# Kernel tuning notes

Hardware: AMD Instinct MI355X
Metric: run time of the kernel (lower is better)

## Reference

```python
import jax, jax.numpy as jnp
import numpy as np

ALPHA = 0.2          # LeakyReLU negative slope
NEG_BIG = -9e15      # mask value from original code


def setup_inputs() -> dict:
    key = jax.random.key(0)
    k1, k2, k3, k4 = jax.random.split(key, 4)
    B, N, F_in, F_out = 16, 1024, 256, 256
    x = jax.random.normal(k1, (B, N, F_in), dtype=jnp.float32)
    adj = jax.random.randint(k2, (B, N, N), 0, 2, dtype=jnp.int32)
    # xavier-uniform-like scales
    W = jax.random.normal(k3, (F_in, F_out), dtype=jnp.float32) * np.sqrt(2.0 / (F_in + F_out))
    a = jax.random.normal(k4, (2 * F_out, 1), dtype=jnp.float32) * np.sqrt(2.0 / (2 * F_out + 1))
    return {"x": x, "adj": adj, "W": W, "a": a}


def reference(x, adj, W, a):
    # x: [B,N,Fin], adj: [B,N,N] (int mask), W: [Fin,Fout], a: [2*Fout,1]
    F_out = a.shape[0] // 2
    h = jnp.einsum("bni,io->bno", x, W)            # [B,N,Fout]
    # Decompose a into left/right halves: e_ij = lrelu(a_l.h_i + a_r.h_j)
    a_l = a[:F_out, 0]                               # [Fout]
    a_r = a[F_out:, 0]                               # [Fout]
    el = h @ a_l                                     # [B,N] score contribution of target i
    er = h @ a_r                                     # [B,N] score contribution of source j
    e = jax.nn.leaky_relu(el[:, :, None] + er[:, None, :], ALPHA)  # [B,N,N]
    e = jnp.where(adj > 0, e, NEG_BIG)
    attn = jax.nn.softmax(e, axis=-1)                # masked softmax over neighbors j
    # weighted sum of neighbor features; concat with n_heads=1 is identity
    return jnp.einsum("bij,bjo->bio", attn, h)       # [B,N,Fout]
```

## Files before the change

kernel.cpp:

```cpp
#include <hip/hip_runtime.h>
#include <stdint.h>

#define ALPHA 0.2f
#define L2E 1.4426950408889634f

typedef __attribute__((ext_vector_type(8))) short bf16x8;
typedef __attribute__((ext_vector_type(4))) float f32x4;

__device__ __forceinline__ unsigned short f2bf(float f) {
    unsigned int u = __float_as_uint(f);
    u += 0x7fffu + ((u >> 16) & 1u);
    return (unsigned short)(u >> 16);
}

__device__ __forceinline__ void gload_lds16(const void* g, void* l) {
    __builtin_amdgcn_global_load_lds(
        (const __attribute__((address_space(1))) unsigned int*)g,
        (__attribute__((address_space(3))) unsigned int*)l, 16, 0, 0);
}

__global__ void wt_wa_kernel(const float* __restrict__ W,
                             const float* __restrict__ a,
                             unsigned short* __restrict__ Wtbf,
                             float* __restrict__ wa) {
    const int t = threadIdx.x;
    if (blockIdx.x < 256) {
        const int o = blockIdx.x;
        Wtbf[o * 256 + t] = f2bf(W[t * 256 + o]);
    } else {
        float sl = 0.f, sr = 0.f;
        const float* wr = W + t * 256;
        for (int o = 0; o < 256; ++o) {
            const float wv = wr[o];
            sl += wv * a[o];
            sr += wv * a[256 + o];
        }
        wa[t] = sl;
        wa[256 + t] = sr;
    }
}

__global__ __launch_bounds__(256) void eler2x_kernel(
    const float* __restrict__ x, const float* __restrict__ wa,
    float* __restrict__ el, float* __restrict__ er,
    unsigned short* __restrict__ xbf)
{
    const int w = threadIdx.x >> 6, l = threadIdx.x & 63;
    const int r = blockIdx.x * 4 + w;
    const float4 xv = *(const float4*)(x + (size_t)r * 256 + l * 4);
    const float4 al = *(const float4*)(wa + l * 4);
    const float4 ar = *(const float4*)(wa + 256 + l * 4);

    ushort4 xb;
    xb.x = f2bf(xv.x); xb.y = f2bf(xv.y); xb.z = f2bf(xv.z); xb.w = f2bf(xv.w);
    *(ushort4*)(xbf + (size_t)r * 256 + l * 4) = xb;

    float sl = xv.x * al.x + xv.y * al.y + xv.z * al.z + xv.w * al.w;
    float sr = xv.x * ar.x + xv.y * ar.y + xv.z * ar.z + xv.w * ar.w;
#pragma unroll
    for (int off = 32; off >= 1; off >>= 1) {
        sl += __shfl_xor(sl, off);
        sr += __shfl_xor(sr, off);
    }
    if (l == 0) { el[r] = sl * L2E; er[r] = sr * L2E; }
}

__global__ __launch_bounds__(256) void gemm_h(
    const unsigned short* __restrict__ A,
    const unsigned short* __restrict__ Bt,
    unsigned short* __restrict__ C)
{
    __shared__ __align__(16) unsigned short As[2 * 64 * 64];
    __shared__ __align__(16) unsigned short Bs[2 * 128 * 64];

    const int tid = threadIdx.x;
    const int w = tid >> 6, l = tid & 63;
    const int q = l >> 4, ml = l & 15;
    const int wm = (w >> 1) * 32;
    const int wn = (w & 1) * 64;
    const int m0 = blockIdx.y * 64;
    const int n0 = blockIdx.x * 128;

    f32x4 acc[2][4];
#pragma unroll
    for (int i = 0; i < 2; ++i)
#pragma unroll
        for (int j = 0; j < 4; ++j) {
            f32x4 z = {0.f, 0.f, 0.f, 0.f};
            acc[i][j] = z;
        }

#define GSTAGE(BI, K0) do {                                                   \
    _Pragma("unroll")                                                         \
    for (int c_ = 0; c_ < 2; ++c_) {                                          \
        const int cb_ = c_ * 256 + (w << 6);                                  \
        const int p_ = cb_ + l;                                               \
        const int r_ = p_ >> 3;                                               \
        const int cc_ = (p_ & 7) ^ (r_ & 7);                                  \
        gload_lds16(A + (size_t)(m0 + r_) * 256 + (K0) + cc_ * 8,             \
                    As + (BI) * 4096 + cb_ * 8);                              \
    }                                                                         \
    _Pragma("unroll")                                                         \
    for (int c_ = 0; c_ < 4; ++c_) {                                          \
        const int cb_ = c_ * 256 + (w << 6);                                  \
        const int p_ = cb_ + l;                                               \
        const int r_ = p_ >> 3;                                               \
        const int cc_ = (p_ & 7) ^ (r_ & 7);                                  \
        gload_lds16(Bt + (size_t)(n0 + r_) * 256 + (K0) + cc_ * 8,            \
                    Bs + (BI) * 8192 + cb_ * 8);                              \
    } } while (0)

    GSTAGE(0, 0);

    for (int s = 0; s < 4; ++s) {
        const int cur = s & 1;
        if (s + 1 < 4) {
            GSTAGE((s + 1) & 1, (s + 1) * 64);
            asm volatile("s_waitcnt vmcnt(6) lgkmcnt(0)" ::: "memory");
        } else {
            asm volatile("s_waitcnt vmcnt(0) lgkmcnt(0)" ::: "memory");
        }
        __builtin_amdgcn_s_barrier();
        __builtin_amdgcn_sched_barrier(0);

        const unsigned short* Ab = As + cur * 4096;
        const unsigned short* Bb = Bs + cur * 8192;
        bf16x8 aF[2][2], bF[2][4];
#pragma unroll
        for (int ks = 0; ks < 2; ++ks) {
#pragma unroll
            for (int mt = 0; mt < 2; ++mt) {
                const int mm = wm + mt * 16 + ml;
                aF[ks][mt] = *(const bf16x8*)(As + cur * 4096 + (mm * 8 + ((ks * 4 + q) ^ (mm & 7))) * 8);
            }
#pragma unroll
            for (int nt = 0; nt < 4; ++nt) {
                const int nn = wn + nt * 16 + ml;
                bF[ks][nt] = *(const bf16x8*)(Bb + (nn * 8 + ((ks * 4 + q) ^ (nn & 7))) * 8);
            }
        }
#pragma unroll
        for (int ks = 0; ks < 2; ++ks)
            for (int mt = 0; mt < 2; ++mt)
                for (int nt = 0; nt < 4; ++nt)
                    acc[mt][nt] = __builtin_amdgcn_mfma_f32_16x16x32_bf16(
                        aF[ks][mt], bF[ks][nt], acc[mt][nt], 0, 0, 0);

        asm volatile("s_waitcnt lgkmcnt(0)" ::: "memory");
        __builtin_amdgcn_s_barrier();
    }
#undef GSTAGE

    for (int mt = 0; mt < 2; ++mt)
        for (int nt = 0; nt < 4; ++nt) {
            const int gn = n0 + wn + nt * 16 + ml;
            for (int r = 0; r < 4; ++r) {
                const int gm = m0 + wm + mt * 16 + q * 4 + r;
                C[(size_t)gm * 16384 + gn] = f2bf(acc[mt][nt][r]);
            }
        }
}

__global__ __launch_bounds__(256) void pbuild_kernel(
    const int* __restrict__ adj,
    const float* __restrict__ el2,
    const float* __restrict__ er2,
    unsigned short* __restrict__ P,
    float* __restrict__ s)
{
    const int w = threadIdx.x >> 6, l = threadIdx.x & 63;
    const int row = blockIdx.x * 4 + w;
    const int b = row >> 10;
    const int* arow = adj + (size_t)row * 1024;
    const float* erb = er2 + (b << 10);
    const float el2i = el2[row];

    float sden = 0.f;
#pragma unroll
    for (int it = 0; it < 4; ++it) {
        const int j = it * 256 + l * 4;
        const int4 av = *(const int4*)(arow + j);
        const float4 erv = *(const float4*)(erb + j);
        float e0 = el2i + erv.x; e0 = fmaxf(e0, ALPHA * e0);
        float e1 = el2i + erv.y; e1 = fmaxf(e1, ALPHA * e1);
        float e2 = el2i + erv.z; e2 = fmaxf(e2, ALPHA * e2);
        float e3 = el2i + erv.w; e3 = fmaxf(e3, ALPHA * e3);
        ushort4 pv;
        pv.x = (av.x > 0) ? f2bf(exp2f(e0)) : (unsigned short)0;
        pv.y = (av.y > 0) ? f2bf(exp2f(e1)) : (unsigned short)0;
        pv.z = (av.z > 0) ? f2bf(exp2f(e2)) : (unsigned short)0;
        pv.w = (av.w > 0) ? f2bf(exp2f(e3)) : (unsigned short)0;
        sden += __uint_as_float((unsigned)pv.x << 16);
        sden += __uint_as_float((unsigned)pv.y << 16);
        sden += __uint_as_float((unsigned)pv.z << 16);
        sden += __uint_as_float((unsigned)pv.w << 16);
        *(ushort4*)(P + (size_t)row * 1024 + j) = pv;
    }
#pragma unroll
    for (int off = 32; off >= 1; off >>= 1) sden += __shfl_xor(sden, off);
    if (l == 0) s[row] = sden;
}

__global__ __launch_bounds__(256) void pvgemm_kernel(
    const unsigned short* __restrict__ P,
    const unsigned short* __restrict__ hT,
    const float* __restrict__ s,
    float* __restrict__ out)
{
    __shared__ __align__(16) unsigned short As[2 * 64 * 64];
    __shared__ __align__(16) unsigned short Bs[2 * 128 * 64];

    const int tid = threadIdx.x;
    const int w = tid >> 6, l = tid & 63;
    const int q = l >> 4, ml = l & 15;
    const int wm = (w >> 1) * 32;
    const int wn = (w & 1) * 64;

    const int bid = blockIdx.x;
    const int slot = bid >> 3;
    const int b = ((bid & 7) << 1) | (slot >> 5);
    const int rem = slot & 31;
    const int n0 = (rem & 1) * 128;
    const int m0 = (rem >> 1) * 64;

    const unsigned short* A = P + ((size_t)b << 20);
    const unsigned short* Bt = hT + ((size_t)b << 10);

    f32x4 acc[2][4];
#pragma unroll
    for (int i = 0; i < 2; ++i)
#pragma unroll
        for (int j = 0; j < 4; ++j) {
            f32x4 z = {0.f, 0.f, 0.f, 0.f};
            acc[i][j] = z;
        }

#define GSTAGE(BI, K0) do {                                                   \
    _Pragma("unroll")                                                         \
    for (int c_ = 0; c_ < 2; ++c_) {                                          \
        const int cb_ = c_ * 256 + (w << 6);                                  \
        const int p_ = cb_ + l;                                               \
        const int r_ = p_ >> 3;                                               \
        const int cc_ = (p_ & 7) ^ (r_ & 7);                                  \
        gload_lds16(A + (size_t)(m0 + r_) * 1024 + (K0) + cc_ * 8,            \
                    As + (BI) * 4096 + cb_ * 8);                              \
    }                                                                         \
    _Pragma("unroll")                                                         \
    for (int c_ = 0; c_ < 4; ++c_) {                                          \
        const int cb_ = c_ * 256 + (w << 6);                                  \
        const int p_ = cb_ + l;                                               \
        const int r_ = p_ >> 3;                                               \
        const int cc_ = (p_ & 7) ^ (r_ & 7);                                  \
        gload_lds16(Bt + (size_t)(n0 + r_) * 16384 + (K0) + cc_ * 8,          \
                    Bs + (BI) * 8192 + cb_ * 8);                              \
    } } while (0)

    GSTAGE(0, 0);

    for (int ks0 = 0; ks0 < 16; ++ks0) {
        const int cur = ks0 & 1;
        if (ks0 + 1 < 16) {
            GSTAGE((ks0 + 1) & 1, (ks0 + 1) * 64);
            asm volatile("s_waitcnt vmcnt(6) lgkmcnt(0)" ::: "memory");
        } else {
            asm volatile("s_waitcnt vmcnt(0) lgkmcnt(0)" ::: "memory");
        }
        __builtin_amdgcn_s_barrier();
        __builtin_amdgcn_sched_barrier(0);

        const unsigned short* Ab = As + cur * 4096;
        const unsigned short* Bb = Bs + cur * 8192;
        bf16x8 aF[2][2], bF[2][4];
#pragma unroll
        for (int ks = 0; ks < 2; ++ks) {
#pragma unroll
            for (int mt = 0; mt < 2; ++mt) {
                const int mm = wm + mt * 16 + ml;
                aF[ks][mt] = *(const bf16x8*)(Ab + (mm * 8 + ((ks * 4 + q) ^ (mm & 7))) * 8);
            }
#pragma unroll
            for (int nt = 0; nt < 4; ++nt) {
                const int nn = wn + nt * 16 + ml;
                bF[ks][nt] = *(const bf16x8*)(Bb + (nn * 8 + ((ks * 4 + q) ^ (nn & 7))) * 8);
            }
        }
        __builtin_amdgcn_s_setprio(1);
#pragma unroll
        for (int ks = 0; ks < 2; ++ks)
            for (int mt = 0; mt < 2; ++mt)
                for (int nt = 0; nt < 4; ++nt)
                    acc[mt][nt] = __builtin_amdgcn_mfma_f32_16x16x32_bf16(
                        aF[ks][mt], bF[ks][nt], acc[mt][nt], 0, 0, 0);
        __builtin_amdgcn_s_setprio(0);

        asm volatile("s_waitcnt lgkmcnt(0)" ::: "memory");
        __builtin_amdgcn_s_barrier();
    }
#undef GSTAGE

    float* ob = out + (size_t)b * 262144;
    const float* sb = s + (b << 10);
#pragma unroll
    for (int mt = 0; mt < 2; ++mt) {
        float rinv[4];
#pragma unroll
        for (int r = 0; r < 4; ++r)
            rinv[r] = 1.0f / sb[m0 + wm + mt * 16 + q * 4 + r];
#pragma unroll
        for (int nt = 0; nt < 4; ++nt) {
            const int gn = n0 + wn + nt * 16 + ml;
#pragma unroll
            for (int r = 0; r < 4; ++r) {
                const int gm = m0 + wm + mt * 16 + q * 4 + r;
                ob[(size_t)gm * 256 + gn] = acc[mt][nt][r] * rinv[r];
            }
        }
    }
}

__global__ __launch_bounds__(512) void maskpv_kernel(
    const int* __restrict__ adj,
    const float* __restrict__ el2,
    const float* __restrict__ er2,
    const unsigned short* __restrict__ hT,
    float* __restrict__ out)
{
    __shared__ float er_s[1024];
    __shared__ float c_s[32];
    __shared__ __align__(16) unsigned short Hs[2 * 256 * 64];
    __shared__ __align__(16) unsigned short Ps[2 * 32 * 72];

    const int tid = threadIdx.x;
    const int w = tid >> 6, l = tid & 63;
    const int q = l >> 4, ml = l & 15;
    const int wm = (w >> 2) * 16;
    const int wn = (w & 3) * 64;

    const int bid = blockIdx.x;
    const int slot = bid >> 3;
    const int b = ((bid & 7) << 1) | (slot >> 5);
    const int i0 = (slot & 31) * 32;

    const int ib = tid >> 4;
    const int js = (tid & 15) * 4;
    const int rg = (b << 10) + i0 + ib;
    const float el2i = el2[rg];

    const unsigned short* hb = hT + (size_t)b * 1024;

#define STAGE(BI, T) do {                                                     \
    const int jb_ = (T) * 64;                                                 \
    _Pragma("unroll")                                                         \
    for (int c_ = 0; c_ < 4; ++c_) {                                          \
        const int cb_ = c_ * 512 + tid;                                       \
        const int r_ = cb_ >> 3;                                              \
        const int cc_ = (cb_ & 7) ^ (r_ & 7);                                 \
        gload_lds16(hb + (size_t)r_ * 16384 + jb_ + cc_ * 8,                  \
                    Hs + (BI) * 16384 + (cb_ << 3));                          \
    } } while (0)

    STAGE(0, 0);

    *(float2*)(er_s + tid * 2) = *(const float2*)(er2 + (b << 10) + tid * 2);
    asm volatile("s_waitcnt lgkmcnt(0)" ::: "memory");
    __builtin_amdgcn_s_barrier();

    unsigned mw0 = 0, mw1 = 0;
    float m1 = -3.0e38f;
    const int* arow = adj + (size_t)rg * 1024 + js;
#pragma unroll
    for (int k = 0; k < 16; ++k) {
        const int4 av = *(const int4*)(arow + k * 64);
        const float4 erv = *(const float4*)(er_s + k * 64 + js);
        float e0 = el2i + erv.x; e0 = fmaxf(e0, ALPHA * e0);
        float e1 = el2i + erv.y; e1 = fmaxf(e1, ALPHA * e1);
        float e2 = el2i + erv.z; e2 = fmaxf(e2, ALPHA * e2);
        float e3 = el2i + erv.w; e3 = fmaxf(e3, ALPHA * e3);
        const unsigned bits = (av.x > 0 ? 1u : 0u) | (av.y > 0 ? 2u : 0u) |
                              (av.z > 0 ? 4u : 0u) | (av.w > 0 ? 8u : 0u);
        e0 = av.x > 0 ? e0 : -3.0e38f;
        e1 = av.y > 0 ? e1 : -3.0e38f;
        e2 = av.z > 0 ? e2 : -3.0e38f;
        e3 = av.w > 0 ? e3 : -3.0e38f;
        m1 = fmaxf(m1, fmaxf(fmaxf(e0, e1), fmaxf(e2, e3)));
        if (k < 8) mw0 |= bits << (k * 4); else mw1 |= bits << ((k - 8) * 4);
    }
#pragma unroll
    for (int off = 1; off <= 8; off <<= 1) m1 = fmaxf(m1, __shfl_xor(m1, off));

    float s0 = 0.f, s1 = 0.f, s2 = 0.f, s3 = 0.f;
#pragma unroll
    for (int k = 0; k < 16; ++k) {
        const float4 erv = *(const float4*)(er_s + k * 64 + js);
        const unsigned mv = ((k < 8) ? (mw0 >> (k * 4)) : (mw1 >> ((k - 8) * 4))) & 0xFu;
        float e0 = el2i + erv.x; e0 = fmaxf(e0, ALPHA * e0);
        float e1 = el2i + erv.y; e1 = fmaxf(e1, ALPHA * e1);
        float e2 = el2i + erv.z; e2 = fmaxf(e2, ALPHA * e2);
        float e3 = el2i + erv.w; e3 = fmaxf(e3, ALPHA * e3);
        s0 += (mv & 1u) ? exp2f(e0 - m1) : 0.f;
        s1 += (mv & 2u) ? exp2f(e1 - m1) : 0.f;
        s2 += (mv & 4u) ? exp2f(e2 - m1) : 0.f;
        s3 += (mv & 8u) ? exp2f(e3 - m1) : 0.f;
    }
    float ssum = (s0 + s1) + (s2 + s3);
#pragma unroll
    for (int off = 1; off <= 8; off <<= 1) ssum += __shfl_xor(ssum, off);
    if ((tid & 15) == 0) c_s[ib] = m1 + log2f(ssum);
    asm volatile("s_waitcnt lgkmcnt(0)" ::: "memory");
    __builtin_amdgcn_s_barrier();
    const float c2i = c_s[ib];

    f32x4 acc[4];
#pragma unroll
    for (int j = 0; j < 4; ++j) {
        f32x4 z = {0.f, 0.f, 0.f, 0.f};
        acc[j] = z;
    }

#define BUILDR(BI, T) do {                                                    \
    const float4 ev_ = *(const float4*)(er_s + (T) * 64 + js);                \
    const unsigned mv_ =                                                      \
        (((T) < 8) ? (mw0 >> ((T) * 4)) : (mw1 >> (((T) - 8) * 4))) & 0xFu;   \
    float e0_ = el2i + ev_.x; e0_ = fmaxf(e0_, ALPHA * e0_);                  \
    float e1_ = el2i + ev_.y; e1_ = fmaxf(e1_, ALPHA * e1_);                  \
    float e2_ = el2i + ev_.z; e2_ = fmaxf(e2_, ALPHA * e2_);                  \
    float e3_ = el2i + ev_.w; e3_ = fmaxf(e3_, ALPHA * e3_);                  \
    ushort4 pv_;                                                              \
    pv_.x = (mv_ & 1u) ? f2bf(exp2f(e0_ - c2i)) : (unsigned short)0;          \
    pv_.y = (mv_ & 2u) ? f2bf(exp2f(e1_ - c2i)) : (unsigned short)0;          \
    pv_.z = (mv_ & 4u) ? f2bf(exp2f(e2_ - c2i)) : (unsigned short)0;          \
    pv_.w = (mv_ & 8u) ? f2bf(exp2f(e3_ - c2i)) : (unsigned short)0;          \
    *(ushort4*)(Ps + (BI) * 2304 + ib * 72 + js) = pv_;                       \
    } while (0)

#define COMPUTE(BI) do {                                                      \
    bf16x8 aF_[2], bF_[2][4];                                                 \
    _Pragma("unroll")                                                         \
    for (int ks_ = 0; ks_ < 2; ++ks_)                                         \
        aF_[ks_] = *(const bf16x8*)(Ps + (BI) * 2304 +                        \
                                    (wm + ml) * 72 + ks_ * 32 + q * 8);       \
    _Pragma("unroll")                                                         \
    for (int ks_ = 0; ks_ < 2; ++ks_)                                         \
        _Pragma("unroll")                                                     \
        for (int nt_ = 0; nt_ < 4; ++nt_) {                                   \
            const int oc_ = wn + nt_ * 16 + ml;                               \
            const int sl_ = (ks_ * 4 + q) ^ (oc_ & 7);                        \
            bF_[ks_][nt_] = *(const bf16x8*)(Hs + (BI) * 16384 +              \
                                             oc_ * 64 + sl_ * 8);             \
        }                                                                     \
    _Pragma("unroll")                                                         \
    for (int ks_ = 0; ks_ < 2; ++ks_)                                         \
        _Pragma("unroll")                                                     \
        for (int nt_ = 0; nt_ < 4; ++nt_)                                     \
            acc[nt_] = __builtin_amdgcn_mfma_f32_16x16x32_bf16(               \
                aF_[ks_], bF_[ks_][nt_], acc[nt_], 0, 0, 0);                  \
    } while (0)

#pragma unroll
    for (int t = 0; t < 16; ++t) {
        const int cur = t & 1;
        if (t + 1 < 16) STAGE((t + 1) & 1, t + 1);
        BUILDR(cur, t);
        if (t + 1 < 16)
            asm volatile("s_waitcnt vmcnt(4) lgkmcnt(0)" ::: "memory");
        else
            asm volatile("s_waitcnt vmcnt(0) lgkmcnt(0)" ::: "memory");
        __builtin_amdgcn_s_barrier();
        __builtin_amdgcn_sched_barrier(0);
        COMPUTE(cur);
        asm volatile("s_waitcnt lgkmcnt(0)" ::: "memory");
        __builtin_amdgcn_s_barrier();
    }

#undef STAGE
#undef BUILDR
#undef COMPUTE

    float* ob = out + (size_t)b * 262144;
#pragma unroll
    for (int nt = 0; nt < 4; ++nt) {
        const int gn = wn + nt * 16 + ml;
#pragma unroll
        for (int r = 0; r < 4; ++r) {
            const int gm = i0 + wm + q * 4 + r;
            ob[(size_t)gm * 256 + gn] = acc[nt][r];
        }
    }
}

extern "C" void kernel_launch(void* const* d_in, const int* in_sizes, int n_in,
                              void* d_out, int out_size, void* d_ws, size_t ws_size,
                              hipStream_t stream) {
    const float* x   = (const float*)d_in[0];
    const int*   adj = (const int*)d_in[1];
    const float* W   = (const float*)d_in[2];
    const float* a   = (const float*)d_in[3];
    float* out = (float*)d_out;

    char* ws = (char*)d_ws;
    unsigned short* Wtbf  = (unsigned short*)(ws);
    float* wa             = (float*)(ws + 131072);
    unsigned short* xbf   = (unsigned short*)(ws + 133120);
    unsigned short* h_T   = (unsigned short*)(ws + 8521728);
    float* el             = (float*)(ws + 16910336);
    float* er             = (float*)(ws + 16975872);
    unsigned short* P     = (unsigned short*)(ws + 17041408);
    float* sden           = (float*)(ws + 50595840);

    wt_wa_kernel<<<dim3(257), dim3(256), 0, stream>>>(W, a, Wtbf, wa);

    eler2x_kernel<<<dim3(4096), dim3(256), 0, stream>>>(x, wa, el, er, xbf);

    gemm_h<<<dim3(128, 4), dim3(256), 0, stream>>>(Wtbf, xbf, h_T);

    if (ws_size >= (size_t)50661376) {
        pbuild_kernel<<<dim3(4096), dim3(256), 0, stream>>>(adj, el, er, P, sden);
        pvgemm_kernel<<<dim3(512), dim3(256), 0, stream>>>(P, h_T, sden, out);
    } else {
        maskpv_kernel<<<dim3(512), dim3(512), 0, stream>>>(adj, el, er, h_T, out);
    }
}
```

Before: 160.1 us.

## Merge h GEMM and P-build into one launch with block-range dispatch

Combines the h = x·W GEMM (512 blocks) and the masked exp P-building pass (4096 blocks) into one kernel, picking the branch by block index. The two are independent, so the compute-bound GEMM can run alongside the memory-bound adjacency streaming, and one launch plus its inter-kernel gap goes away. In exchange the P-build blocks now reserve the GEMM's shared memory, which may lower their occupancy. There is also a small cleanup that uses the Ab pointer in gemm_h.

```diff
diff --git a/kernel.cpp b/kernel.cpp
--- a/kernel.cpp
+++ b/kernel.cpp
@@ -131,7 +131,7 @@
 #pragma unroll
             for (int mt = 0; mt < 2; ++mt) {
                 const int mm = wm + mt * 16 + ml;
-                aF[ks][mt] = *(const bf16x8*)(As + cur * 4096 + (mm * 8 + ((ks * 4 + q) ^ (mm & 7))) * 8);
+                aF[ks][mt] = *(const bf16x8*)(Ab + (mm * 8 + ((ks * 4 + q) ^ (mm & 7))) * 8);
             }
 #pragma unroll
             for (int nt = 0; nt < 4; ++nt) {
@@ -161,44 +161,139 @@
         }
 }
 
-__global__ __launch_bounds__(256) void pbuild_kernel(
+__global__ __launch_bounds__(256) void gemm_pbuild_kernel(
+    const unsigned short* __restrict__ A,
+    const unsigned short* __restrict__ Bt,
+    unsigned short* __restrict__ C,
     const int* __restrict__ adj,
     const float* __restrict__ el2,
     const float* __restrict__ er2,
     unsigned short* __restrict__ P,
     float* __restrict__ s)
 {
-    const int w = threadIdx.x >> 6, l = threadIdx.x & 63;
-    const int row = blockIdx.x * 4 + w;
-    const int b = row >> 10;
-    const int* arow = adj + (size_t)row * 1024;
-    const float* erb = er2 + (b << 10);
-    const float el2i = el2[row];
-
-    float sden = 0.f;
-#pragma unroll
-    for (int it = 0; it < 4; ++it) {
-        const int j = it * 256 + l * 4;
-        const int4 av = *(const int4*)(arow + j);
-        const float4 erv = *(const float4*)(erb + j);
-        float e0 = el2i + erv.x; e0 = fmaxf(e0, ALPHA * e0);
-        float e1 = el2i + erv.y; e1 = fmaxf(e1, ALPHA * e1);
-        float e2 = el2i + erv.z; e2 = fmaxf(e2, ALPHA * e2);
-        float e3 = el2i + erv.w; e3 = fmaxf(e3, ALPHA * e3);
-        ushort4 pv;
-        pv.x = (av.x > 0) ? f2bf(exp2f(e0)) : (unsigned short)0;
-        pv.y = (av.y > 0) ? f2bf(exp2f(e1)) : (unsigned short)0;
-        pv.z = (av.z > 0) ? f2bf(exp2f(e2)) : (unsigned short)0;
-        pv.w = (av.w > 0) ? f2bf(exp2f(e3)) : (unsigned short)0;
-        sden += __uint_as_float((unsigned)pv.x << 16);
-        sden += __uint_as_float((unsigned)pv.y << 16);
-        sden += __uint_as_float((unsigned)pv.z << 16);
-        sden += __uint_as_float((unsigned)pv.w << 16);
-        *(ushort4*)(P + (size_t)row * 1024 + j) = pv;
-    }
-#pragma unroll
-    for (int off = 32; off >= 1; off >>= 1) sden += __shfl_xor(sden, off);
-    if (l == 0) s[row] = sden;
+    __shared__ __align__(16) unsigned short As[2 * 64 * 64];
+    __shared__ __align__(16) unsigned short Bs[2 * 128 * 64];
+
+    const int tid = threadIdx.x;
+    const int w = tid >> 6, l = tid & 63;
+
+    if (blockIdx.x < 512) {
+        const int q = l >> 4, ml = l & 15;
+        const int wm = (w >> 1) * 32;
+        const int wn = (w & 1) * 64;
+        const int m0 = (blockIdx.x >> 7) * 64;
+        const int n0 = (blockIdx.x & 127) * 128;
+
+        f32x4 acc[2][4];
+#pragma unroll
+        for (int i = 0; i < 2; ++i)
+#pragma unroll
+            for (int j = 0; j < 4; ++j) {
+                f32x4 z = {0.f, 0.f, 0.f, 0.f};
+                acc[i][j] = z;
+            }
+
+#define GSTAGE(BI, K0) do {                                                   \
+    _Pragma("unroll")                                                         \
+    for (int c_ = 0; c_ < 2; ++c_) {                                          \
+        const int cb_ = c_ * 256 + (w << 6);                                  \
+        const int p_ = cb_ + l;                                               \
+        const int r_ = p_ >> 3;                                               \
+        const int cc_ = (p_ & 7) ^ (r_ & 7);                                  \
+        gload_lds16(A + (size_t)(m0 + r_) * 256 + (K0) + cc_ * 8,             \
+                    As + (BI) * 4096 + cb_ * 8);                              \
+    }                                                                         \
+    _Pragma("unroll")                                                         \
+    for (int c_ = 0; c_ < 4; ++c_) {                                          \
+        const int cb_ = c_ * 256 + (w << 6);                                  \
+        const int p_ = cb_ + l;                                               \
+        const int r_ = p_ >> 3;                                               \
+        const int cc_ = (p_ & 7) ^ (r_ & 7);                                  \
+        gload_lds16(Bt + (size_t)(n0 + r_) * 256 + (K0) + cc_ * 8,            \
+                    Bs + (BI) * 8192 + cb_ * 8);                              \
+    } } while (0)
+
+        GSTAGE(0, 0);
+
+        for (int st = 0; st < 4; ++st) {
+            const int cur = st & 1;
+            if (st + 1 < 4) {
+                GSTAGE((st + 1) & 1, (st + 1) * 64);
+                asm volatile("s_waitcnt vmcnt(6) lgkmcnt(0)" ::: "memory");
+            } else {
+                asm volatile("s_waitcnt vmcnt(0) lgkmcnt(0)" ::: "memory");
+            }
+            __builtin_amdgcn_s_barrier();
+            __builtin_amdgcn_sched_barrier(0);
+
+            const unsigned short* Ab = As + cur * 4096;
+            const unsigned short* Bb = Bs + cur * 8192;
+            bf16x8 aF[2][2], bF[2][4];
+#pragma unroll
+            for (int ks = 0; ks < 2; ++ks) {
+#pragma unroll
+                for (int mt = 0; mt < 2; ++mt) {
+                    const int mm = wm + mt * 16 + ml;
+                    aF[ks][mt] = *(const bf16x8*)(Ab + (mm * 8 + ((ks * 4 + q) ^ (mm & 7))) * 8);
+                }
+#pragma unroll
+                for (int nt = 0; nt < 4; ++nt) {
+                    const int nn = wn + nt * 16 + ml;
+                    bF[ks][nt] = *(const bf16x8*)(Bb + (nn * 8 + ((ks * 4 + q) ^ (nn & 7))) * 8);
+                }
+            }
+#pragma unroll
+            for (int ks = 0; ks < 2; ++ks)
+                for (int mt = 0; mt < 2; ++mt)
+                    for (int nt = 0; nt < 4; ++nt)
+                        acc[mt][nt] = __builtin_amdgcn_mfma_f32_16x16x32_bf16(
+                            aF[ks][mt], bF[ks][nt], acc[mt][nt], 0, 0, 0);
+
+            asm volatile("s_waitcnt lgkmcnt(0)" ::: "memory");
+            __builtin_amdgcn_s_barrier();
+        }
+#undef GSTAGE
+
+        for (int mt = 0; mt < 2; ++mt)
+            for (int nt = 0; nt < 4; ++nt) {
+                const int gn = n0 + wn + nt * 16 + ml;
+                for (int r = 0; r < 4; ++r) {
+                    const int gm = m0 + wm + mt * 16 + q * 4 + r;
+                    C[(size_t)gm * 16384 + gn] = f2bf(acc[mt][nt][r]);
+                }
+            }
+    } else {
+        const int row = (blockIdx.x - 512) * 4 + w;
+        const int b = row >> 10;
+        const int* arow = adj + (size_t)row * 1024;
+        const float* erb = er2 + (b << 10);
+        const float el2i = el2[row];
+
+        float sden = 0.f;
+#pragma unroll
+        for (int it = 0; it < 4; ++it) {
+            const int j = it * 256 + l * 4;
+            const int4 av = *(const int4*)(arow + j);
+            const float4 erv = *(const float4*)(erb + j);
+            float e0 = el2i + erv.x; e0 = fmaxf(e0, ALPHA * e0);
+            float e1 = el2i + erv.y; e1 = fmaxf(e1, ALPHA * e1);
+            float e2 = el2i + erv.z; e2 = fmaxf(e2, ALPHA * e2);
+            float e3 = el2i + erv.w; e3 = fmaxf(e3, ALPHA * e3);
+            ushort4 pv;
+            pv.x = (av.x > 0) ? f2bf(exp2f(e0)) : (unsigned short)0;
+            pv.y = (av.y > 0) ? f2bf(exp2f(e1)) : (unsigned short)0;
+            pv.z = (av.z > 0) ? f2bf(exp2f(e2)) : (unsigned short)0;
+            pv.w = (av.w > 0) ? f2bf(exp2f(e3)) : (unsigned short)0;
+            sden += __uint_as_float((unsigned)pv.x << 16);
+            sden += __uint_as_float((unsigned)pv.y << 16);
+            sden += __uint_as_float((unsigned)pv.z << 16);
+            sden += __uint_as_float((unsigned)pv.w << 16);
+            *(ushort4*)(P + (size_t)row * 1024 + j) = pv;
+        }
+#pragma unroll
+        for (int off = 32; off >= 1; off >>= 1) sden += __shfl_xor(sden, off);
+        if (l == 0) s[row] = sden;
+    }
 }
 
 __global__ __launch_bounds__(256) void pvgemm_kernel(
@@ -511,12 +606,12 @@
 
     eler2x_kernel<<<dim3(4096), dim3(256), 0, stream>>>(x, wa, el, er, xbf);
 
-    gemm_h<<<dim3(128, 4), dim3(256), 0, stream>>>(Wtbf, xbf, h_T);
-
     if (ws_size >= (size_t)50661376) {
-        pbuild_kernel<<<dim3(4096), dim3(256), 0, stream>>>(adj, el, er, P, sden);
+        gemm_pbuild_kernel<<<dim3(4608), dim3(256), 0, stream>>>(
+            Wtbf, xbf, h_T, adj, el, er, P, sden);
         pvgemm_kernel<<<dim3(512), dim3(256), 0, stream>>>(P, h_T, sden, out);
     } else {
+        gemm_h<<<dim3(128, 4), dim3(256), 0, stream>>>(Wtbf, xbf, h_T);
         maskpv_kernel<<<dim3(512), dim3(512), 0, stream>>>(adj, el, er, h_T, out);
     }
 }
```

Result: slower. 167.5 us (+4.6%).
